# Kernel tuning notes

Measured on AMD Instinct MI355X. Metric: run time of the kernel, lower is better.

The kernel has to match this reference:

```python
import jax, jax.numpy as jnp
import numpy as np

N_RAYS = 32768
N_SAMPLES = 2097152  # ~64 samples/ray after occupancy-grid culling
HIDDEN = 64
STEP = 0.005  # render_step_size


def setup_inputs() -> dict:
    key = jax.random.key(0)
    ks = jax.random.split(key, 8)
    rays_o = jax.random.normal(ks[0], (N_RAYS, 3), jnp.float32)
    rays_d = jax.random.normal(ks[1], (N_RAYS, 3), jnp.float32)
    rays_d = rays_d / jnp.linalg.norm(rays_d, axis=-1, keepdims=True)
    W1 = jax.random.normal(ks[2], (3, HIDDEN), jnp.float32) * 0.5
    b1 = jnp.zeros((HIDDEN,), jnp.float32)
    W2 = jax.random.normal(ks[3], (HIDDEN, 1), jnp.float32) * 0.1
    b2 = jnp.zeros((1,), jnp.float32)
    # sorted ray indices (occGrid.sampling emits samples grouped by ray)
    ray_indices = jnp.sort(jax.random.randint(ks[4], (N_SAMPLES,), 0, N_RAYS, jnp.int32))
    t_starts = jax.random.uniform(ks[5], (N_SAMPLES,), jnp.float32, 0.2, 2.0)
    t_ends = t_starts + STEP
    return {"rays_o": rays_o, "rays_d": rays_d, "W1": W1, "b1": b1,
            "W2": W2, "b2": b2, "t_starts": t_starts, "t_ends": t_ends,
            "ray_indices": ray_indices, "n_rays": N_RAYS}


def reference(rays_o, rays_d, W1, b1, W2, b2, t_starts, t_ends, ray_indices, n_rays):
    # sigma_fn: gather ray origins/dirs per sample, evaluate density MLP at midpoints
    t_mid = (t_starts + t_ends) * 0.5                       # [S]
    positions = rays_o[ray_indices] + rays_d[ray_indices] * t_mid[:, None]  # [S,3]
    h = jax.nn.relu(positions @ W1 + b1)                    # [S,H]
    sigmas = jax.nn.softplus((h @ W2 + b2)[:, 0])           # [S]

    # render_weight_from_density: per-ray exclusive cumsum of sigma*dt
    s = sigmas * (t_ends - t_starts)                        # [S]
    cum = jnp.cumsum(s)
    excl = cum - s                                          # global exclusive cumsum
    # first sample index of each ray (ray_indices is sorted)
    first_idx = jnp.searchsorted(ray_indices, jnp.arange(n_rays, dtype=ray_indices.dtype))
    offset = excl[first_idx[ray_indices]]                   # exclusive-cumsum at segment start
    trans = jnp.exp(-(excl - offset))                       # per-ray transmittance
    alphas = 1.0 - jnp.exp(-s)
    weights = trans * alphas                                # [S]

    # accumulate_along_rays: segment reductions over rays
    opacities = jax.ops.segment_sum(weights, ray_indices, num_segments=n_rays)
    depth_num = jax.ops.segment_sum(weights * t_mid, ray_indices, num_segments=n_rays)
    depths = depth_num / jnp.clip(opacities, jnp.finfo(opacities.dtype).tiny)
    return jnp.stack([opacities, depths], axis=-1)          # [n_rays, 2]
```

## Files before the change

### kernel.cpp

```cpp
#include <hip/hip_runtime.h>
#include <math.h>

#define HIDDEN 64

typedef _Float16 half8   __attribute__((ext_vector_type(8)));
typedef _Float16 half2_t __attribute__((ext_vector_type(2)));
typedef float    f32x16  __attribute__((ext_vector_type(16)));
typedef int      int4_t  __attribute__((ext_vector_type(4)));

template <int CTRL, int RMASK>
__device__ __forceinline__ float dpp_add(float v) {
    int t = __builtin_amdgcn_update_dpp(0, __builtin_bit_cast(int, v),
                                        CTRL, RMASK, 0xF, true);
    return v + __builtin_bit_cast(float, t);
}

__device__ __forceinline__ float bcast_lane(float v, int lane) {
    return __builtin_bit_cast(float,
        __builtin_amdgcn_readlane(__builtin_bit_cast(int, v), lane));
}

__device__ __forceinline__ half2_t pack2(float a, float b) {
    return __builtin_bit_cast(half2_t, __builtin_amdgcn_cvt_pkrtz(a, b));
}

__device__ __forceinline__ half2_t pk_relu(half2_t h) {
    half2_t r;
    asm("v_pk_max_f16 %0, %1, 0" : "=v"(r) : "v"(h));
    return r;
}

__device__ __forceinline__ float scan32(float v) {
    v = dpp_add<0x111, 0xF>(v);
    v = dpp_add<0x112, 0xF>(v);
    v = dpp_add<0x114, 0xF>(v);
    v = dpp_add<0x118, 0xF>(v);
    v = dpp_add<0x142, 0xA>(v);
    return v;
}

__global__ __launch_bounds__(256) void seg_bounds_kernel(
    const int* __restrict__ ray_indices, int* __restrict__ first_idx,
    int n_samples, int n_rays)
{
    const int i = blockIdx.x * blockDim.x + threadIdx.x;
    if (i >= n_samples) return;
    const int cur  = ray_indices[i];
    const int prev = (i == 0) ? -1 : ray_indices[i - 1];
    for (int r = prev + 1; r <= cur; ++r) first_idx[r] = i;
    if (i == n_samples - 1) {
        for (int r = cur + 1; r < n_rays; ++r) first_idx[r] = n_samples;
    }
}

__global__ __launch_bounds__(256, 4) void nerf_render_kernel(
    const float* __restrict__ rays_o, const float* __restrict__ rays_d,
    const float* __restrict__ W1, const float* __restrict__ b1,
    const float* __restrict__ W2, const float* __restrict__ b2,
    const float* __restrict__ t_starts,
    const int* __restrict__ first_idx,
    float* __restrict__ out, int n_rays, int n_samples)
{
    const int tid  = threadIdx.x;
    const int lane = tid & 63;
    const int ray  = (blockIdx.x * blockDim.x + tid) >> 6;
    if (ray >= n_rays) return;

    const int n = lane & 31;
    const int q = lane >> 5;

    half8 a0 = {}, a1 = {};
    if (q == 0) {
        const int m = n;
        a0[0] = (_Float16)W1[0 * HIDDEN + m];
        a0[1] = (_Float16)W1[1 * HIDDEN + m];
        a0[2] = (_Float16)W1[2 * HIDDEN + m];
        a0[3] = (_Float16)b1[m];
        a1[0] = (_Float16)W1[0 * HIDDEN + 32 + m];
        a1[1] = (_Float16)W1[1 * HIDDEN + 32 + m];
        a1[2] = (_Float16)W1[2 * HIDDEN + 32 + m];
        a1[3] = (_Float16)b1[32 + m];
    }

    half2_t w2a[8], w2b[8];
    #pragma unroll
    for (int r8 = 0; r8 < 8; ++r8) {
        const int row = 2 * (r8 & 1) + 8 * (r8 >> 1) + 4 * q;
        half2_t pa, pb;
        pa[0] = (_Float16)W2[row];      pa[1] = (_Float16)W2[row + 1];
        pb[0] = (_Float16)W2[row + 32]; pb[1] = (_Float16)W2[row + 33];
        w2a[r8] = pa; w2b[r8] = pb;
    }
    const float bias2 = b2[0];

    const int seg_start = first_idx[ray];
    const int seg_end   = (ray + 1 < n_rays) ? first_idx[ray + 1] : n_samples;
    if (seg_start >= seg_end) {
        if (lane == 0) { out[2 * ray] = 0.0f; out[2 * ray + 1] = 0.0f; }
        return;
    }

    const float ox = rays_o[3 * ray + 0];
    const float oy = rays_o[3 * ray + 1];
    const float oz = rays_o[3 * ray + 2];
    const float dx = rays_d[3 * ray + 0];
    const float dy = rays_d[3 * ray + 1];
    const float dz = rays_d[3 * ray + 2];

    const int xaddr = (lane ^ 32) << 2;
    const int bmask = (q == 0) ? ~0 : 0;

    float carry = 0.0f, op_acc = 0.0f, depth_acc = 0.0f;

    const int last = seg_end - 1;
    const int ia = seg_start + n;
    const int ib = ia + 32;
    float tsa = t_starts[(ia < seg_end) ? ia : last];
    float tsb = t_starts[(ib < seg_end) ? ib : last];

    const f32x16 zc = {};

    for (int base = seg_start; base < seg_end; base += 64) {
        const bool va = (base + n      < seg_end);
        const bool vb = (base + 32 + n < seg_end);
        const float ts_a = tsa;
        const float ts_b = tsb;

        const float tm_a = ts_a + 0.0025f;
        const float tm_b = ts_b + 0.0025f;
        const float dt   = 0.005f;

        const float pxa = fmaf(dx, tm_a, ox);
        const float pya = fmaf(dy, tm_a, oy);
        const float pza = fmaf(dz, tm_a, oz);
        const float pxb = fmaf(dx, tm_b, ox);
        const float pyb = fmaf(dy, tm_b, oy);
        const float pzb = fmaf(dz, tm_b, oz);

        const int a01 = __builtin_bit_cast(int, __builtin_amdgcn_cvt_pkrtz(pxa, pya)) & bmask;
        const int a23 = __builtin_bit_cast(int, __builtin_amdgcn_cvt_pkrtz(pza, 1.0f)) & bmask;
        const int b01 = __builtin_bit_cast(int, __builtin_amdgcn_cvt_pkrtz(pxb, pyb)) & bmask;
        const int b23 = __builtin_bit_cast(int, __builtin_amdgcn_cvt_pkrtz(pzb, 1.0f)) & bmask;
        const int4_t bia = {a01, a23, 0, 0};
        const int4_t bib = {b01, b23, 0, 0};
        const half8 bfa = __builtin_bit_cast(half8, bia);
        const half8 bfb = __builtin_bit_cast(half8, bib);

        {
            const int nxa = base + 64 + n;
            const int nxb = base + 96 + n;
            tsa = t_starts[(nxa < seg_end) ? nxa : last];
            tsb = t_starts[(nxb < seg_end) ? nxb : last];
        }

        float z_a, z_b;
        {
            const f32x16 d0 = __builtin_amdgcn_mfma_f32_32x32x16_f16(a0, bfa, zc, 0, 0, 0);
            const f32x16 d1 = __builtin_amdgcn_mfma_f32_32x32x16_f16(a1, bfa, zc, 0, 0, 0);
            float c0 = 0.0f, c1 = 0.0f, c2 = 0.0f, c3 = 0.0f;
            #pragma unroll
            for (int r8 = 0; r8 < 8; r8 += 4) {
                c0 = __builtin_amdgcn_fdot2(pk_relu(pack2(d0[2*r8+0], d0[2*r8+1])), w2a[r8+0], c0, false);
                c1 = __builtin_amdgcn_fdot2(pk_relu(pack2(d0[2*r8+2], d0[2*r8+3])), w2a[r8+1], c1, false);
                c2 = __builtin_amdgcn_fdot2(pk_relu(pack2(d0[2*r8+4], d0[2*r8+5])), w2a[r8+2], c2, false);
                c3 = __builtin_amdgcn_fdot2(pk_relu(pack2(d0[2*r8+6], d0[2*r8+7])), w2a[r8+3], c3, false);
            }
            #pragma unroll
            for (int r8 = 0; r8 < 8; r8 += 4) {
                c0 = __builtin_amdgcn_fdot2(pk_relu(pack2(d1[2*r8+0], d1[2*r8+1])), w2b[r8+0], c0, false);
                c1 = __builtin_amdgcn_fdot2(pk_relu(pack2(d1[2*r8+2], d1[2*r8+3])), w2b[r8+1], c1, false);
                c2 = __builtin_amdgcn_fdot2(pk_relu(pack2(d1[2*r8+4], d1[2*r8+5])), w2b[r8+2], c2, false);
                c3 = __builtin_amdgcn_fdot2(pk_relu(pack2(d1[2*r8+6], d1[2*r8+7])), w2b[r8+3], c3, false);
            }
            const float acc = (c0 + c1) + (c2 + c3);
            const int oth = __builtin_amdgcn_ds_bpermute(xaddr, __builtin_bit_cast(int, acc));
            z_a = acc + __builtin_bit_cast(float, oth) + bias2;
        }
        {
            const f32x16 d0 = __builtin_amdgcn_mfma_f32_32x32x16_f16(a0, bfb, zc, 0, 0, 0);
            const f32x16 d1 = __builtin_amdgcn_mfma_f32_32x32x16_f16(a1, bfb, zc, 0, 0, 0);
            float c0 = 0.0f, c1 = 0.0f, c2 = 0.0f, c3 = 0.0f;
            #pragma unroll
            for (int r8 = 0; r8 < 8; r8 += 4) {
                c0 = __builtin_amdgcn_fdot2(pk_relu(pack2(d0[2*r8+0], d0[2*r8+1])), w2a[r8+0], c0, false);
                c1 = __builtin_amdgcn_fdot2(pk_relu(pack2(d0[2*r8+2], d0[2*r8+3])), w2a[r8+1], c1, false);
                c2 = __builtin_amdgcn_fdot2(pk_relu(pack2(d0[2*r8+4], d0[2*r8+5])), w2a[r8+2], c2, false);
                c3 = __builtin_amdgcn_fdot2(pk_relu(pack2(d0[2*r8+6], d0[2*r8+7])), w2a[r8+3], c3, false);
            }
            #pragma unroll
            for (int r8 = 0; r8 < 8; r8 += 4) {
                c0 = __builtin_amdgcn_fdot2(pk_relu(pack2(d1[2*r8+0], d1[2*r8+1])), w2b[r8+0], c0, false);
                c1 = __builtin_amdgcn_fdot2(pk_relu(pack2(d1[2*r8+2], d1[2*r8+3])), w2b[r8+1], c1, false);
                c2 = __builtin_amdgcn_fdot2(pk_relu(pack2(d1[2*r8+4], d1[2*r8+5])), w2b[r8+2], c2, false);
                c3 = __builtin_amdgcn_fdot2(pk_relu(pack2(d1[2*r8+6], d1[2*r8+7])), w2b[r8+3], c3, false);
            }
            const float acc = (c0 + c1) + (c2 + c3);
            const int oth = __builtin_amdgcn_ds_bpermute(xaddr, __builtin_bit_cast(int, acc));
            z_b = acc + __builtin_bit_cast(float, oth) + bias2;
        }

        const float sg_a = fmaxf(z_a, 0.0f) + __logf(1.0f + __expf(-fabsf(z_a)));
        const float sg_b = fmaxf(z_b, 0.0f) + __logf(1.0f + __expf(-fabsf(z_b)));
        const float sv_a = va ? sg_a * dt : 0.0f;
        const float sv_b = vb ? sg_b * dt : 0.0f;

        const float sc_a  = scan32(sv_a);
        const float sc_b  = scan32(sv_b);
        const float tot_a = bcast_lane(sc_a, 31);

        const float incl_a = carry + sc_a;
        const float incl_b = carry + tot_a + sc_b;
        const float w_a = __expf(sv_a - incl_a) - __expf(-incl_a);
        const float w_b = __expf(sv_b - incl_b) - __expf(-incl_b);

        op_acc    += w_a + w_b;
        depth_acc  = fmaf(w_a, tm_a, fmaf(w_b, tm_b, depth_acc));
        carry     += tot_a + bcast_lane(sc_b, 31);
    }

    const float op_tot = bcast_lane(scan32(op_acc), 31);
    const float dp_tot = bcast_lane(scan32(depth_acc), 31);

    if (lane == 0) {
        const float tiny = 1.17549435e-38f;
        out[2 * ray + 0] = op_tot;
        out[2 * ray + 1] = dp_tot / fmaxf(op_tot, tiny);
    }
}

extern "C" void kernel_launch(void* const* d_in, const int* in_sizes, int n_in,
                              void* d_out, int out_size, void* d_ws, size_t ws_size,
                              hipStream_t stream) {
    const float* rays_o      = (const float*)d_in[0];
    const float* rays_d      = (const float*)d_in[1];
    const float* W1          = (const float*)d_in[2];
    const float* b1          = (const float*)d_in[3];
    const float* W2          = (const float*)d_in[4];
    const float* b2          = (const float*)d_in[5];
    const float* t_starts    = (const float*)d_in[6];
    const int*   ray_indices = (const int*)d_in[8];

    const int n_rays    = in_sizes[0] / 3;
    const int n_samples = in_sizes[6];

    float* out       = (float*)d_out;
    int*   first_idx = (int*)d_ws;

    {
        const int block = 256;
        const int grid  = (n_samples + block - 1) / block;
        seg_bounds_kernel<<<grid, block, 0, stream>>>(ray_indices, first_idx,
                                                      n_samples, n_rays);
    }
    {
        const int block = 256;
        const int grid  = (n_rays * 64 + block - 1) / block;
        nerf_render_kernel<<<grid, block, 0, stream>>>(
            rays_o, rays_d, W1, b1, W2, b2, t_starts, first_idx,
            out, n_rays, n_samples);
    }
}
```

Measured before the change: 119.0 us.

## Split density MLP into flat sample-parallel kernel and separate per-ray scan

Moves the MLP evaluation out of the per-ray loop into a kernel where each wave handles a fixed chunk of 512 samples, gathering ray origin and direction per sample, and writes sigma*dt to a workspace buffer. The segment-boundary computation is folded into this kernel. A second lightweight kernel does the per-ray exclusive scan using a full 64-lane DPP scan over the stored values. This aims to remove load imbalance and tail waste from ray-parallel MLP work, at the cost of an extra global write and read of a per-sample array and per-sample gathers of ray data.

```diff
diff --git a/kernel.cpp b/kernel.cpp
--- a/kernel.cpp
+++ b/kernel.cpp
@@ -2,6 +2,8 @@
 #include <math.h>
 
 #define HIDDEN 64
+#define WAVE_SAMPLES 512
+#define SVAL_OFFSET 262144
 
 typedef _Float16 half8   __attribute__((ext_vector_type(8)));
 typedef _Float16 half2_t __attribute__((ext_vector_type(2)));
@@ -30,44 +32,59 @@
     return r;
 }
 
-__device__ __forceinline__ float scan32(float v) {
+__device__ __forceinline__ float scan64(float v) {
     v = dpp_add<0x111, 0xF>(v);
     v = dpp_add<0x112, 0xF>(v);
     v = dpp_add<0x114, 0xF>(v);
     v = dpp_add<0x118, 0xF>(v);
     v = dpp_add<0x142, 0xA>(v);
+    v = dpp_add<0x143, 0xC>(v);
     return v;
 }
 
-__global__ __launch_bounds__(256) void seg_bounds_kernel(
-    const int* __restrict__ ray_indices, int* __restrict__ first_idx,
-    int n_samples, int n_rays)
-{
-    const int i = blockIdx.x * blockDim.x + threadIdx.x;
-    if (i >= n_samples) return;
-    const int cur  = ray_indices[i];
-    const int prev = (i == 0) ? -1 : ray_indices[i - 1];
-    for (int r = prev + 1; r <= cur; ++r) first_idx[r] = i;
-    if (i == n_samples - 1) {
-        for (int r = cur + 1; r < n_rays; ++r) first_idx[r] = n_samples;
-    }
-}
-
-__global__ __launch_bounds__(256, 4) void nerf_render_kernel(
+__device__ __forceinline__ float mlp_z(half8 a0, half8 a1,
+                                       const half2_t* w2a, const half2_t* w2b,
+                                       half8 bf, int xaddr, float bias2) {
+    const f32x16 zc = {};
+    const f32x16 d0 = __builtin_amdgcn_mfma_f32_32x32x16_f16(a0, bf, zc, 0, 0, 0);
+    const f32x16 d1 = __builtin_amdgcn_mfma_f32_32x32x16_f16(a1, bf, zc, 0, 0, 0);
+    float c0 = 0.0f, c1 = 0.0f, c2 = 0.0f, c3 = 0.0f;
+    #pragma unroll
+    for (int r8 = 0; r8 < 8; r8 += 4) {
+        c0 = __builtin_amdgcn_fdot2(pk_relu(pack2(d0[2*r8+0], d0[2*r8+1])), w2a[r8+0], c0, false);
+        c1 = __builtin_amdgcn_fdot2(pk_relu(pack2(d0[2*r8+2], d0[2*r8+3])), w2a[r8+1], c1, false);
+        c2 = __builtin_amdgcn_fdot2(pk_relu(pack2(d0[2*r8+4], d0[2*r8+5])), w2a[r8+2], c2, false);
+        c3 = __builtin_amdgcn_fdot2(pk_relu(pack2(d0[2*r8+6], d0[2*r8+7])), w2a[r8+3], c3, false);
+    }
+    #pragma unroll
+    for (int r8 = 0; r8 < 8; r8 += 4) {
+        c0 = __builtin_amdgcn_fdot2(pk_relu(pack2(d1[2*r8+0], d1[2*r8+1])), w2b[r8+0], c0, false);
+        c1 = __builtin_amdgcn_fdot2(pk_relu(pack2(d1[2*r8+2], d1[2*r8+3])), w2b[r8+1], c1, false);
+        c2 = __builtin_amdgcn_fdot2(pk_relu(pack2(d1[2*r8+4], d1[2*r8+5])), w2b[r8+2], c2, false);
+        c3 = __builtin_amdgcn_fdot2(pk_relu(pack2(d1[2*r8+6], d1[2*r8+7])), w2b[r8+3], c3, false);
+    }
+    const float acc = (c0 + c1) + (c2 + c3);
+    const int oth = __builtin_amdgcn_ds_bpermute(xaddr, __builtin_bit_cast(int, acc));
+    return acc + __builtin_bit_cast(float, oth) + bias2;
+}
+
+__global__ __launch_bounds__(256, 4) void mlp_density_kernel(
     const float* __restrict__ rays_o, const float* __restrict__ rays_d,
     const float* __restrict__ W1, const float* __restrict__ b1,
     const float* __restrict__ W2, const float* __restrict__ b2,
-    const float* __restrict__ t_starts,
-    const int* __restrict__ first_idx,
-    float* __restrict__ out, int n_rays, int n_samples)
+    const float* __restrict__ t_starts, const int* __restrict__ ray_indices,
+    float* __restrict__ sval_out, int* __restrict__ first_idx,
+    int n_samples, int n_rays)
 {
     const int tid  = threadIdx.x;
     const int lane = tid & 63;
-    const int ray  = (blockIdx.x * blockDim.x + tid) >> 6;
-    if (ray >= n_rays) return;
-
+    const int wave = (blockIdx.x * blockDim.x + tid) >> 6;
     const int n = lane & 31;
     const int q = lane >> 5;
+
+    const int base0 = wave * WAVE_SAMPLES;
+    if (base0 >= n_samples) return;
+    const int lim = (base0 + WAVE_SAMPLES < n_samples) ? (base0 + WAVE_SAMPLES) : n_samples;
 
     half8 a0 = {}, a1 = {};
     if (q == 0) {
@@ -81,7 +98,6 @@
         a1[2] = (_Float16)W1[2 * HIDDEN + 32 + m];
         a1[3] = (_Float16)b1[32 + m];
     }
-
     half2_t w2a[8], w2b[8];
     #pragma unroll
     for (int r8 = 0; r8 < 8; ++r8) {
@@ -92,50 +108,46 @@
         w2a[r8] = pa; w2b[r8] = pb;
     }
     const float bias2 = b2[0];
-
-    const int seg_start = first_idx[ray];
-    const int seg_end   = (ray + 1 < n_rays) ? first_idx[ray + 1] : n_samples;
-    if (seg_start >= seg_end) {
-        if (lane == 0) { out[2 * ray] = 0.0f; out[2 * ray + 1] = 0.0f; }
-        return;
-    }
-
-    const float ox = rays_o[3 * ray + 0];
-    const float oy = rays_o[3 * ray + 1];
-    const float oz = rays_o[3 * ray + 2];
-    const float dx = rays_d[3 * ray + 0];
-    const float dy = rays_d[3 * ray + 1];
-    const float dz = rays_d[3 * ray + 2];
-
     const int xaddr = (lane ^ 32) << 2;
     const int bmask = (q == 0) ? ~0 : 0;
 
-    float carry = 0.0f, op_acc = 0.0f, depth_acc = 0.0f;
-
-    const int last = seg_end - 1;
-    const int ia = seg_start + n;
-    const int ib = ia + 32;
-    float tsa = t_starts[(ia < seg_end) ? ia : last];
-    float tsb = t_starts[(ib < seg_end) ? ib : last];
-
-    const f32x16 zc = {};
-
-    for (int base = seg_start; base < seg_end; base += 64) {
-        const bool va = (base + n      < seg_end);
-        const bool vb = (base + 32 + n < seg_end);
-        const float ts_a = tsa;
-        const float ts_b = tsb;
-
-        const float tm_a = ts_a + 0.0025f;
-        const float tm_b = ts_b + 0.0025f;
-        const float dt   = 0.005f;
-
-        const float pxa = fmaf(dx, tm_a, ox);
-        const float pya = fmaf(dy, tm_a, oy);
-        const float pza = fmaf(dz, tm_a, oz);
-        const float pxb = fmaf(dx, tm_b, ox);
-        const float pyb = fmaf(dy, tm_b, oy);
-        const float pzb = fmaf(dz, tm_b, oz);
+    for (int base = base0; base < lim; base += 64) {
+        const int iS = base + lane;
+        if (iS < n_samples) {
+            const int cur  = ray_indices[iS];
+            const int prev = (iS == 0) ? -1 : ray_indices[iS - 1];
+            for (int r = prev + 1; r <= cur; ++r) first_idx[r] = iS;
+            if (iS == n_samples - 1) {
+                for (int r = cur + 1; r < n_rays; ++r) first_idx[r] = n_samples;
+            }
+        }
+
+        const int ia = base + n;
+        const int ib = ia + 32;
+        const bool va = (ia < n_samples);
+        const bool vb = (ib < n_samples);
+        const int ca = va ? ia : (n_samples - 1);
+        const int cb = vb ? ib : (n_samples - 1);
+
+        const float tsa = t_starts[ca];
+        const float tsb = t_starts[cb];
+        const int   ria = ray_indices[ca];
+        const int   rib = ray_indices[cb];
+
+        const float tm_a = tsa + 0.0025f;
+        const float tm_b = tsb + 0.0025f;
+
+        const float oxa = rays_o[3 * ria + 0], oya = rays_o[3 * ria + 1], oza = rays_o[3 * ria + 2];
+        const float dxa = rays_d[3 * ria + 0], dya = rays_d[3 * ria + 1], dza = rays_d[3 * ria + 2];
+        const float oxb = rays_o[3 * rib + 0], oyb = rays_o[3 * rib + 1], ozb = rays_o[3 * rib + 2];
+        const float dxb = rays_d[3 * rib + 0], dyb = rays_d[3 * rib + 1], dzb = rays_d[3 * rib + 2];
+
+        const float pxa = fmaf(dxa, tm_a, oxa);
+        const float pya = fmaf(dya, tm_a, oya);
+        const float pza = fmaf(dza, tm_a, oza);
+        const float pxb = fmaf(dxb, tm_b, oxb);
+        const float pyb = fmaf(dyb, tm_b, oyb);
+        const float pzb = fmaf(dzb, tm_b, ozb);
 
         const int a01 = __builtin_bit_cast(int, __builtin_amdgcn_cvt_pkrtz(pxa, pya)) & bmask;
         const int a23 = __builtin_bit_cast(int, __builtin_amdgcn_cvt_pkrtz(pza, 1.0f)) & bmask;
@@ -143,83 +155,59 @@
         const int b23 = __builtin_bit_cast(int, __builtin_amdgcn_cvt_pkrtz(pzb, 1.0f)) & bmask;
         const int4_t bia = {a01, a23, 0, 0};
         const int4_t bib = {b01, b23, 0, 0};
-        const half8 bfa = __builtin_bit_cast(half8, bia);
-        const half8 bfb = __builtin_bit_cast(half8, bib);
-
-        {
-            const int nxa = base + 64 + n;
-            const int nxb = base + 96 + n;
-            tsa = t_starts[(nxa < seg_end) ? nxa : last];
-            tsb = t_starts[(nxb < seg_end) ? nxb : last];
-        }
-
-        float z_a, z_b;
-        {
-            const f32x16 d0 = __builtin_amdgcn_mfma_f32_32x32x16_f16(a0, bfa, zc, 0, 0, 0);
-            const f32x16 d1 = __builtin_amdgcn_mfma_f32_32x32x16_f16(a1, bfa, zc, 0, 0, 0);
-            float c0 = 0.0f, c1 = 0.0f, c2 = 0.0f, c3 = 0.0f;
-            #pragma unroll
-            for (int r8 = 0; r8 < 8; r8 += 4) {
-                c0 = __builtin_amdgcn_fdot2(pk_relu(pack2(d0[2*r8+0], d0[2*r8+1])), w2a[r8+0], c0, false);
-                c1 = __builtin_amdgcn_fdot2(pk_relu(pack2(d0[2*r8+2], d0[2*r8+3])), w2a[r8+1], c1, false);
-                c2 = __builtin_amdgcn_fdot2(pk_relu(pack2(d0[2*r8+4], d0[2*r8+5])), w2a[r8+2], c2, false);
-                c3 = __builtin_amdgcn_fdot2(pk_relu(pack2(d0[2*r8+6], d0[2*r8+7])), w2a[r8+3], c3, false);
-            }
-            #pragma unroll
-            for (int r8 = 0; r8 < 8; r8 += 4) {
-                c0 = __builtin_amdgcn_fdot2(pk_relu(pack2(d1[2*r8+0], d1[2*r8+1])), w2b[r8+0], c0, false);
-                c1 = __builtin_amdgcn_fdot2(pk_relu(pack2(d1[2*r8+2], d1[2*r8+3])), w2b[r8+1], c1, false);
-                c2 = __builtin_amdgcn_fdot2(pk_relu(pack2(d1[2*r8+4], d1[2*r8+5])), w2b[r8+2], c2, false);
-                c3 = __builtin_amdgcn_fdot2(pk_relu(pack2(d1[2*r8+6], d1[2*r8+7])), w2b[r8+3], c3, false);
-            }
-            const float acc = (c0 + c1) + (c2 + c3);
-            const int oth = __builtin_amdgcn_ds_bpermute(xaddr, __builtin_bit_cast(int, acc));
-            z_a = acc + __builtin_bit_cast(float, oth) + bias2;
-        }
-        {
-            const f32x16 d0 = __builtin_amdgcn_mfma_f32_32x32x16_f16(a0, bfb, zc, 0, 0, 0);
-            const f32x16 d1 = __builtin_amdgcn_mfma_f32_32x32x16_f16(a1, bfb, zc, 0, 0, 0);
-            float c0 = 0.0f, c1 = 0.0f, c2 = 0.0f, c3 = 0.0f;
-            #pragma unroll
-            for (int r8 = 0; r8 < 8; r8 += 4) {
-                c0 = __builtin_amdgcn_fdot2(pk_relu(pack2(d0[2*r8+0], d0[2*r8+1])), w2a[r8+0], c0, false);
-                c1 = __builtin_amdgcn_fdot2(pk_relu(pack2(d0[2*r8+2], d0[2*r8+3])), w2a[r8+1], c1, false);
-                c2 = __builtin_amdgcn_fdot2(pk_relu(pack2(d0[2*r8+4], d0[2*r8+5])), w2a[r8+2], c2, false);
-                c3 = __builtin_amdgcn_fdot2(pk_relu(pack2(d0[2*r8+6], d0[2*r8+7])), w2a[r8+3], c3, false);
-            }
-            #pragma unroll
-            for (int r8 = 0; r8 < 8; r8 += 4) {
-                c0 = __builtin_amdgcn_fdot2(pk_relu(pack2(d1[2*r8+0], d1[2*r8+1])), w2b[r8+0], c0, false);
-                c1 = __builtin_amdgcn_fdot2(pk_relu(pack2(d1[2*r8+2], d1[2*r8+3])), w2b[r8+1], c1, false);
-                c2 = __builtin_amdgcn_fdot2(pk_relu(pack2(d1[2*r8+4], d1[2*r8+5])), w2b[r8+2], c2, false);
-                c3 = __builtin_amdgcn_fdot2(pk_relu(pack2(d1[2*r8+6], d1[2*r8+7])), w2b[r8+3], c3, false);
-            }
-            const float acc = (c0 + c1) + (c2 + c3);
-            const int oth = __builtin_amdgcn_ds_bpermute(xaddr, __builtin_bit_cast(int, acc));
-            z_b = acc + __builtin_bit_cast(float, oth) + bias2;
-        }
+
+        const float z_a = mlp_z(a0, a1, w2a, w2b, __builtin_bit_cast(half8, bia), xaddr, bias2);
+        const float z_b = mlp_z(a0, a1, w2a, w2b, __builtin_bit_cast(half8, bib), xaddr, bias2);
 
         const float sg_a = fmaxf(z_a, 0.0f) + __logf(1.0f + __expf(-fabsf(z_a)));
         const float sg_b = fmaxf(z_b, 0.0f) + __logf(1.0f + __expf(-fabsf(z_b)));
-        const float sv_a = va ? sg_a * dt : 0.0f;
-        const float sv_b = vb ? sg_b * dt : 0.0f;
-
-        const float sc_a  = scan32(sv_a);
-        const float sc_b  = scan32(sv_b);
-        const float tot_a = bcast_lane(sc_a, 31);
-
-        const float incl_a = carry + sc_a;
-        const float incl_b = carry + tot_a + sc_b;
-        const float w_a = __expf(sv_a - incl_a) - __expf(-incl_a);
-        const float w_b = __expf(sv_b - incl_b) - __expf(-incl_b);
-
-        op_acc    += w_a + w_b;
-        depth_acc  = fmaf(w_a, tm_a, fmaf(w_b, tm_b, depth_acc));
-        carry     += tot_a + bcast_lane(sc_b, 31);
-    }
-
-    const float op_tot = bcast_lane(scan32(op_acc), 31);
-    const float dp_tot = bcast_lane(scan32(depth_acc), 31);
+
+        if (q == 0) {
+            if (va) sval_out[ia] = sg_a * 0.005f;
+            if (vb) sval_out[ib] = sg_b * 0.005f;
+        }
+    }
+}
+
+__global__ __launch_bounds__(256, 8) void render_scan_kernel(
+    const float* __restrict__ t_starts, const float* __restrict__ sval,
+    const int* __restrict__ first_idx,
+    float* __restrict__ out, int n_rays, int n_samples)
+{
+    const int tid  = threadIdx.x;
+    const int lane = tid & 63;
+    const int ray  = (blockIdx.x * blockDim.x + tid) >> 6;
+    if (ray >= n_rays) return;
+
+    const int seg_start = first_idx[ray];
+    const int seg_end   = (ray + 1 < n_rays) ? first_idx[ray + 1] : n_samples;
+    if (seg_start >= seg_end) {
+        if (lane == 0) { out[2 * ray] = 0.0f; out[2 * ray + 1] = 0.0f; }
+        return;
+    }
+
+    float carry = 0.0f, op_acc = 0.0f, depth_acc = 0.0f;
+    const int last = seg_end - 1;
+
+    for (int base = seg_start; base < seg_end; base += 64) {
+        const int  i     = base + lane;
+        const bool valid = (i < seg_end);
+        const int  ic    = valid ? i : last;
+
+        const float sv = valid ? sval[ic] : 0.0f;
+        const float tm = t_starts[ic] + 0.0025f;
+
+        const float scan = scan64(sv);
+        const float incl = carry + scan;
+        const float w    = __expf(sv - incl) - __expf(-incl);
+
+        op_acc    += w;
+        depth_acc  = fmaf(w, tm, depth_acc);
+        carry     += bcast_lane(scan, 63);
+    }
+
+    const float op_tot = bcast_lane(scan64(op_acc), 63);
+    const float dp_tot = bcast_lane(scan64(depth_acc), 63);
 
     if (lane == 0) {
         const float tiny = 1.17549435e-38f;
@@ -245,18 +233,18 @@
 
     float* out       = (float*)d_out;
     int*   first_idx = (int*)d_ws;
+    float* sval      = (float*)((char*)d_ws + SVAL_OFFSET);
 
     {
-        const int block = 256;
-        const int grid  = (n_samples + block - 1) / block;
-        seg_bounds_kernel<<<grid, block, 0, stream>>>(ray_indices, first_idx,
-                                                      n_samples, n_rays);
+        const int waves  = (n_samples + WAVE_SAMPLES - 1) / WAVE_SAMPLES;
+        const int blocks = (waves + 3) / 4;
+        mlp_density_kernel<<<blocks, 256, 0, stream>>>(
+            rays_o, rays_d, W1, b1, W2, b2, t_starts, ray_indices,
+            sval, first_idx, n_samples, n_rays);
     }
     {
-        const int block = 256;
-        const int grid  = (n_rays * 64 + block - 1) / block;
-        nerf_render_kernel<<<grid, block, 0, stream>>>(
-            rays_o, rays_d, W1, b1, W2, b2, t_starts, first_idx,
-            out, n_rays, n_samples);
-    }
-}
+        const int blocks = (n_rays * 64 + 255) / 256;
+        render_scan_kernel<<<blocks, 256, 0, stream>>>(
+            t_starts, sval, first_idx, out, n_rays, n_samples);
+    }
+}
```

Result: faster. 112.5 us (-5.5%).
